# Kernel tuning notes

Hardware: AMD Instinct MI355X
Metric: run time of the kernel (lower is better)

The kernel has to match this reference:

```python
import jax, jax.numpy as jnp
import numpy as np

B, S, F = 4, 2048, 512
H, DH, OUT = 8, 64, 512  # attention_dim=512 -> head_dim=64
NEG_SLOPE = 0.01


def setup_inputs() -> dict:
    key = jax.random.key(0)
    ks = jax.random.split(key, 9)
    sc_in = 1.0 / np.sqrt(F)
    sc_hd = 1.0 / np.sqrt(H * DH)
    return {
        "x": jax.random.normal(ks[0], (B, S, F), dtype=jnp.float32),
        "Wq": jax.random.normal(ks[1], (F, H, DH), dtype=jnp.float32) * sc_in,
        "bq": jnp.zeros((H, DH), dtype=jnp.float32),
        "Wk": jax.random.normal(ks[2], (F, H, DH), dtype=jnp.float32) * sc_in,
        "bk": jnp.zeros((H, DH), dtype=jnp.float32),
        "Wv": jax.random.normal(ks[3], (F, H, DH), dtype=jnp.float32) * sc_in,
        "bv": jnp.zeros((H, DH), dtype=jnp.float32),
        "Wo": jax.random.normal(ks[4], (H, DH, OUT), dtype=jnp.float32) * sc_hd,
        "bo": jnp.zeros((OUT,), dtype=jnp.float32),
    }


def reference(x, Wq, bq, Wk, bk, Wv, bv, Wo, bo):
    # QKV projections: DenseGeneral(axis=-1, features=(H, DH)) -> [B, S, H, DH]
    q = jnp.einsum('bsf,fhd->bshd', x, Wq) + bq
    k = jnp.einsum('bsf,fhd->bshd', x, Wk) + bk
    v = jnp.einsum('bsf,fhd->bshd', x, Wv) + bv

    # Pairwise squared L2: l2[b,h,i,j] = ||q[b,i,h]-k[b,j,h]||^2
    q2 = jnp.sum(q * q, axis=-1)              # [B, S, H]
    k2 = jnp.sum(k * k, axis=-1)              # [B, S, H]
    qk = jnp.einsum('bihd,bjhd->bhij', q, k)  # [B, H, S, S]
    l2 = (q2.transpose(0, 2, 1)[:, :, :, None]
          + k2.transpose(0, 2, 1)[:, :, None, :]
          - 2.0 * qk)

    # softmax over key axis j, then weights.T @ value (note the transpose:
    # output token index is j, summed over query index i, as in the original)
    w = jax.nn.softmax(-l2, axis=-1)                  # [B, H, Si, Sj]
    attn = jnp.einsum('bhij,bihd->bjhd', w, v)        # [B, S, H, DH]

    # out DenseGeneral contracting (H, DH)
    out = jnp.einsum('bshd,hdo->bso', attn, Wo) + bo
    return jnp.where(out >= 0, out, NEG_SLOPE * out)
```

## Files before the change

### kernel.cpp

```cpp
#include <hip/hip_runtime.h>


typedef __attribute__((ext_vector_type(8))) short bf16x8;
typedef __attribute__((ext_vector_type(4))) float f32x4;
typedef __attribute__((ext_vector_type(4))) unsigned short u16x4;

#define MFMA16 __builtin_amdgcn_mfma_f32_16x16x32_bf16
#define LOG2E 1.4426950408889634f
#define TWO_LOG2E 2.8853900817779268f

__device__ inline unsigned short f2bf(float f) {
  unsigned int u = __float_as_uint(f);
  unsigned int r = 0x7fffu + ((u >> 16) & 1u);
  return (unsigned short)((u + r) >> 16);
}
__device__ inline float bf2f(unsigned short h) {
  return __uint_as_float(((unsigned int)h) << 16);
}
__device__ inline float fexp2(float x) { return __builtin_amdgcn_exp2f(x); }

__device__ inline void gl_lds16(const unsigned short* g, unsigned short* lds) {
  __builtin_amdgcn_global_load_lds(
      (const __attribute__((address_space(1))) unsigned int*)g,
      (__attribute__((address_space(3))) unsigned int*)lds, 16, 0, 0);
}

#define NXB4 (8192*512/4)
#define NWQ (1536*512)
#define NWO (512*512)

__global__ __launch_bounds__(256) void prep(
    const float* __restrict__ x, const float* __restrict__ Wq,
    const float* __restrict__ Wk, const float* __restrict__ Wv,
    const float* __restrict__ Wo, const float* __restrict__ bq,
    const float* __restrict__ bk, const float* __restrict__ bv,
    unsigned short* __restrict__ xb, unsigned short* __restrict__ wqkvT,
    unsigned short* __restrict__ woT, float* __restrict__ biasp) {
  int i = blockIdx.x * blockDim.x + threadIdx.x;
  if (i < NXB4) {
    f32x4 v = ((const f32x4*)x)[i];
    u16x4 o;
    o.x = f2bf(v.x); o.y = f2bf(v.y); o.z = f2bf(v.z); o.w = f2bf(v.w);
    ((u16x4*)xb)[i] = o;
    return;
  }
  i -= NXB4;
  if (i < NWQ) {
    int n = i >> 9, f = i & 511;
    const float* W = (n < 512) ? Wq : (n < 1024) ? Wk : Wv;
    wqkvT[i] = f2bf(W[f * 512 + (n & 511)]);
    return;
  }
  i -= NWQ;
  if (i < NWO) {
    int o = i >> 9, hd = i & 511;
    woT[i] = f2bf(Wo[hd * 512 + o]);
    return;
  }
  i -= NWO;
  if (i < 1536) {
    biasp[i] = (i < 512) ? bq[i] : (i < 1024) ? bk[i - 512] : bv[i - 1024];
  }
}

template<int MODE>
__global__ __launch_bounds__(256) void gemm_bt(
    const unsigned short* __restrict__ A, const unsigned short* __restrict__ Bt,
    const float* __restrict__ bias,
    unsigned short* __restrict__ o_q, unsigned short* __restrict__ o_k,
    unsigned short* __restrict__ o_v, float* __restrict__ o_f, int K) {
  const int m0 = blockIdx.y * 128;
  const int n0 = blockIdx.x * 128;
  const int tid = threadIdx.x;
  const int w = tid >> 6, l = tid & 63, lg = l >> 4, ll = l & 15;
  const int wr = w >> 1, wc = w & 1;
  __shared__ unsigned short a_lds[128 * 32];
  __shared__ unsigned short b_lds[128 * 32];
  f32x4 acc[4][4] = {};
  const int nkt = K >> 5;
  for (int kt = 0; kt < nkt; ++kt) {
#pragma unroll
    for (int c = 0; c < 2; ++c) {
      const int cc_base = c * 256 + w * 64;
      const int cc = cc_base + l;
      const int row = cc >> 2, cl = cc & 3;
      gl_lds16(A + (size_t)(m0 + row) * K + kt * 32 + cl * 8, a_lds + cc_base * 8);
      gl_lds16(Bt + (size_t)(n0 + row) * K + kt * 32 + cl * 8, b_lds + cc_base * 8);
    }
    __syncthreads();
    bf16x8 af[4], bfr[4];
#pragma unroll
    for (int mi = 0; mi < 4; ++mi)
      af[mi] = *(const bf16x8*)(a_lds + (wr * 64 + mi * 16 + ll) * 32 + lg * 8);
#pragma unroll
    for (int ni = 0; ni < 4; ++ni)
      bfr[ni] = *(const bf16x8*)(b_lds + (wc * 64 + ni * 16 + ll) * 32 + lg * 8);
#pragma unroll
    for (int mi = 0; mi < 4; ++mi)
#pragma unroll
      for (int ni = 0; ni < 4; ++ni)
        acc[mi][ni] = MFMA16(af[mi], bfr[ni], acc[mi][ni], 0, 0, 0);
    __syncthreads();
  }
#pragma unroll
  for (int mi = 0; mi < 4; ++mi)
#pragma unroll
    for (int ni = 0; ni < 4; ++ni) {
      const int col = n0 + wc * 64 + ni * 16 + ll;
      const float bb = bias[col];
#pragma unroll
      for (int r = 0; r < 4; ++r) {
        const int row = m0 + wr * 64 + mi * 16 + lg * 4 + r;
        float v = acc[mi][ni][r] + bb;
        if (MODE == 0) {
          const int which = col >> 9, h = (col >> 6) & 7, d = col & 63;
          const int b = row >> 11, s = row & 2047;
          if (which == 0) v *= TWO_LOG2E;
          const size_t idx = ((size_t)((b * 8 + h) * 2048 + s)) * 64 + d;
          (which == 0 ? o_q : which == 1 ? o_k : o_v)[idx] = f2bf(v);
        } else {
          v = v >= 0.f ? v : 0.01f * v;
          o_f[(size_t)row * 512 + col] = v;
        }
      }
    }
}

__global__ __launch_bounds__(256) void k2_kernel(const unsigned short* __restrict__ k_g,
                                                 float* __restrict__ k2l_g) {
  const int lane = threadIdx.x & 63;
  const int wid = (blockIdx.x * blockDim.x + threadIdx.x) >> 6;
  const int nw = (gridDim.x * blockDim.x) >> 6;
  for (int row = wid; row < 32 * 2048; row += nw) {
    float v = bf2f(k_g[(size_t)row * 64 + lane]);
    v *= v;
#pragma unroll
    for (int m = 1; m < 64; m <<= 1) v += __shfl_xor(v, m);
    if (lane == 0) k2l_g[row] = LOG2E * v;
  }
}

__global__ __launch_bounds__(256) void transpose_v(const unsigned short* __restrict__ v_g,
                                                   const float* __restrict__ invl_g,
                                                   unsigned short* __restrict__ vt_g) {
  const int bh = blockIdx.x >> 5, st = blockIdx.x & 31;
  const int s0 = st * 64;
  __shared__ unsigned short tile[64][72];
  const int t = threadIdx.x;
  {
    const int sl = t >> 2, cg = t & 3;
    const float sc = invl_g[bh * 2048 + s0 + sl];
    const unsigned short* src = v_g + ((size_t)(bh * 2048 + s0 + sl)) * 64 + cg * 16;
    bf16x8 v0 = *(const bf16x8*)(src);
    bf16x8 v1 = *(const bf16x8*)(src + 8);
#pragma unroll
    for (int e = 0; e < 8; ++e) tile[sl][cg * 16 + e] = f2bf(sc * bf2f((unsigned short)v0[e]));
#pragma unroll
    for (int e = 0; e < 8; ++e) tile[sl][cg * 16 + 8 + e] = f2bf(sc * bf2f((unsigned short)v1[e]));
  }
  __syncthreads();
  {
    const int dl = t >> 2, sg = t & 3;
    bf16x8 o0, o1;
#pragma unroll
    for (int e = 0; e < 8; ++e) o0[e] = (short)tile[sg * 16 + e][dl];
#pragma unroll
    for (int e = 0; e < 8; ++e) o1[e] = (short)tile[sg * 16 + 8 + e][dl];
    unsigned short* dst = vt_g + ((size_t)(bh * 64 + dl)) * 2048 + s0 + sg * 16;
    *(bf16x8*)dst = o0;
    *(bf16x8*)(dst + 8) = o1;
  }
}

__global__ __launch_bounds__(256) void pass1(const unsigned short* __restrict__ q_g,
                                             const unsigned short* __restrict__ k_g,
                                             const float* __restrict__ k2l_g,
                                             float* __restrict__ invl_g) {
  const int bh = blockIdx.x >> 5, ib = blockIdx.x & 31;
  const int i0 = ib * 64;
  const int tid = threadIdx.x, w = tid >> 6, l = tid & 63, lg = l >> 4, ll = l & 15;
  __shared__ unsigned short k_lds[64 * 64];
  __shared__ float k2_lds[64];
  const unsigned short* qrow = q_g + ((size_t)(bh * 2048 + i0 + w * 16 + ll)) * 64;
  const bf16x8 qa0 = *(const bf16x8*)(qrow + lg * 8);
  const bf16x8 qa1 = *(const bf16x8*)(qrow + 32 + lg * 8);
  float lrun[4] = {0.f, 0.f, 0.f, 0.f};
  for (int jt = 0; jt < 32; ++jt) {
    const int j0 = jt * 64;
#pragma unroll
    for (int c = 0; c < 2; ++c) {
      const int cc_base = c * 256 + w * 64;
      const int cc = cc_base + l;
      const int row = cc >> 3, cl = cc & 7;
      gl_lds16(k_g + ((size_t)(bh * 2048 + j0 + row)) * 64 + ((cl ^ (row & 7)) * 8),
               k_lds + cc_base * 8);
    }
    if (tid < 64) k2_lds[tid] = k2l_g[bh * 2048 + j0 + tid];
    __syncthreads();
#pragma unroll
    for (int nf = 0; nf < 4; ++nf) {
      const int jr = nf * 16 + ll;
      const unsigned short* kb = k_lds + jr * 64;
      const int sw = jr & 7;
      bf16x8 b0 = *(const bf16x8*)(kb + ((lg ^ sw) * 8));
      bf16x8 b1 = *(const bf16x8*)(kb + (((4 + lg) ^ sw) * 8));
      f32x4 sa = {};
      sa = MFMA16(qa0, b0, sa, 0, 0, 0);
      sa = MFMA16(qa1, b1, sa, 0, 0, 0);
      const float k2v = k2_lds[jr];
      lrun[0] += fexp2(sa[0] - k2v);
      lrun[1] += fexp2(sa[1] - k2v);
      lrun[2] += fexp2(sa[2] - k2v);
      lrun[3] += fexp2(sa[3] - k2v);
    }
    __syncthreads();
  }
#pragma unroll
  for (int r = 0; r < 4; ++r) {
    float t = lrun[r];
#pragma unroll
    for (int m = 1; m < 16; m <<= 1) t += __shfl_xor(t, m);
    if (ll == 0) invl_g[bh * 2048 + i0 + w * 16 + lg * 4 + r] = 1.f / t;
  }
}

__global__ __launch_bounds__(256) void pass2(const unsigned short* __restrict__ q_g,
                                             const unsigned short* __restrict__ k_g,
                                             const unsigned short* __restrict__ vt_g,
                                             const float* __restrict__ k2l_g,
                                             unsigned short* __restrict__ attnb) {
  const int bh = blockIdx.x >> 4, jb = blockIdx.x & 15;
  const int j0 = jb * 128;
  const int tid = threadIdx.x, w = tid >> 6, l = tid & 63, lg = l >> 4, ll = l & 15;
  __shared__ unsigned short q_lds[2][64 * 64];
  __shared__ unsigned short vt_lds[2][64 * 64];
  __shared__ unsigned short p_lds[128 * 64];
  const unsigned short* q_base = q_g + (size_t)bh * 2048 * 64;
  const unsigned short* vt_base = vt_g + (size_t)bh * 64 * 2048;
  const unsigned short* krow = k_g + ((size_t)(bh * 2048 + j0 + w * 32 + ll)) * 64;
  const bf16x8 ka00 = *(const bf16x8*)(krow + lg * 8);
  const bf16x8 ka01 = *(const bf16x8*)(krow + 32 + lg * 8);
  const bf16x8 ka10 = *(const bf16x8*)(krow + 1024 + lg * 8);
  const bf16x8 ka11 = *(const bf16x8*)(krow + 1024 + 32 + lg * 8);
  float k2v0[4], k2v1[4];
#pragma unroll
  for (int r = 0; r < 4; ++r) {
    k2v0[r] = k2l_g[bh * 2048 + j0 + w * 32 + lg * 4 + r];
    k2v1[r] = k2l_g[bh * 2048 + j0 + w * 32 + 16 + lg * 4 + r];
  }
  f32x4 oacc0[4] = {};
  f32x4 oacc1[4] = {};
#pragma unroll
  for (int c = 0; c < 2; ++c) {
    const int cc_base = c * 256 + w * 64;
    const int cc = cc_base + l;
    const int row = cc >> 3, cl = cc & 7;
    const int csw = (cl ^ (row & 7)) * 8;
    gl_lds16(q_base + (size_t)row * 64 + csw, &q_lds[0][cc_base * 8]);
    gl_lds16(vt_base + (size_t)row * 2048 + csw, &vt_lds[0][cc_base * 8]);
  }
  __syncthreads();
  for (int it = 0; it < 32; ++it) {
    const int slot = it & 1;
    if (it + 1 < 32) {
      const int i1 = (it + 1) * 64;
#pragma unroll
      for (int c = 0; c < 2; ++c) {
        const int cc_base = c * 256 + w * 64;
        const int cc = cc_base + l;
        const int row = cc >> 3, cl = cc & 7;
        const int csw = (cl ^ (row & 7)) * 8;
        gl_lds16(q_base + (size_t)(i1 + row) * 64 + csw, &q_lds[slot ^ 1][cc_base * 8]);
        gl_lds16(vt_base + (size_t)row * 2048 + i1 + csw, &vt_lds[slot ^ 1][cc_base * 8]);
      }
    }
#pragma unroll
    for (int nf = 0; nf < 4; ++nf) {
      const int ir = nf * 16 + ll;
      const unsigned short* qb = &q_lds[slot][ir * 64];
      const int sw = ir & 7;
      bf16x8 b0 = *(const bf16x8*)(qb + ((lg ^ sw) * 8));
      bf16x8 b1 = *(const bf16x8*)(qb + (((4 + lg) ^ sw) * 8));
      f32x4 sa0 = {};
      sa0 = MFMA16(ka00, b0, sa0, 0, 0, 0);
      sa0 = MFMA16(ka01, b1, sa0, 0, 0, 0);
      f32x4 sa1 = {};
      sa1 = MFMA16(ka10, b0, sa1, 0, 0, 0);
      sa1 = MFMA16(ka11, b1, sa1, 0, 0, 0);
#pragma unroll
      for (int r = 0; r < 4; ++r) {
        const float p0 = fexp2(sa0[r] - k2v0[r]);
        const float p1 = fexp2(sa1[r] - k2v1[r]);
        const int ja = w * 32 + lg * 4 + r;
        const int jb2 = ja + 16;
        p_lds[ja * 64 + (ir ^ ((ja & 7) << 3))] =
            (unsigned short)(__float_as_uint(p0) >> 16);
        p_lds[jb2 * 64 + (ir ^ ((jb2 & 7) << 3))] =
            (unsigned short)(__float_as_uint(p1) >> 16);
      }
    }
    {
      const int jr0 = w * 32 + ll;
      const int jr1 = jr0 + 16;
      const int swp = ll & 7;
      const unsigned short* pb0 = p_lds + jr0 * 64;
      const unsigned short* pb1 = p_lds + jr1 * 64;
      bf16x8 pa00 = *(const bf16x8*)(pb0 + ((lg ^ swp) * 8));
      bf16x8 pa01 = *(const bf16x8*)(pb0 + (((4 + lg) ^ swp) * 8));
      bf16x8 pa10 = *(const bf16x8*)(pb1 + ((lg ^ swp) * 8));
      bf16x8 pa11 = *(const bf16x8*)(pb1 + (((4 + lg) ^ swp) * 8));
#pragma unroll
      for (int nf = 0; nf < 4; ++nf) {
        const int dr = nf * 16 + ll;
        const unsigned short* vb = &vt_lds[slot][dr * 64];
        const int sw = dr & 7;
        bf16x8 v0 = *(const bf16x8*)(vb + ((lg ^ sw) * 8));
        bf16x8 v1 = *(const bf16x8*)(vb + (((4 + lg) ^ sw) * 8));
        oacc0[nf] = MFMA16(pa00, v0, oacc0[nf], 0, 0, 0);
        oacc0[nf] = MFMA16(pa01, v1, oacc0[nf], 0, 0, 0);
        oacc1[nf] = MFMA16(pa10, v0, oacc1[nf], 0, 0, 0);
        oacc1[nf] = MFMA16(pa11, v1, oacc1[nf], 0, 0, 0);
      }
    }
    __syncthreads();
  }
  const int b = bh >> 3, h2 = bh & 7;
#pragma unroll
  for (int nf = 0; nf < 4; ++nf) {
    const int d = nf * 16 + ll;
#pragma unroll
    for (int r = 0; r < 4; ++r) {
      const int j = j0 + w * 32 + lg * 4 + r;
      attnb[((size_t)(b * 2048 + j)) * 512 + h2 * 64 + d] = f2bf(oacc0[nf][r]);
      attnb[((size_t)(b * 2048 + j + 16)) * 512 + h2 * 64 + d] = f2bf(oacc1[nf][r]);
    }
  }
}

extern "C" void kernel_launch(void* const* d_in, const int* in_sizes, int n_in,
                              void* d_out, int out_size, void* d_ws, size_t ws_size,
                              hipStream_t stream) {
  const float* x  = (const float*)d_in[0];
  const float* Wq = (const float*)d_in[1];
  const float* bq = (const float*)d_in[2];
  const float* Wk = (const float*)d_in[3];
  const float* bk = (const float*)d_in[4];
  const float* Wv = (const float*)d_in[5];
  const float* bv = (const float*)d_in[6];
  const float* Wo = (const float*)d_in[7];
  const float* bo = (const float*)d_in[8];
  float* out = (float*)d_out;
  char* ws = (char*)d_ws;

  unsigned short* xb    = (unsigned short*)(ws);
  unsigned short* wqkvT = (unsigned short*)(ws + 8388608);
  unsigned short* woT   = (unsigned short*)(ws + 9961472);
  float*          biasp = (float*)         (ws + 10485760);
  unsigned short* q_g   = (unsigned short*)(ws + 10493952);
  unsigned short* k_g   = (unsigned short*)(ws + 18882560);
  unsigned short* v_g   = (unsigned short*)(ws + 27271168);
  unsigned short* vt_g  = (unsigned short*)(ws + 35659776);
  float*          k2_g  = (float*)         (ws + 44048384);
  float*          invl_g= (float*)         (ws + 44310528);
  unsigned short* attnb = (unsigned short*)(ws + 44572672);
  if (ws_size < (size_t)52961280) return;

  prep<<<8199, 256, 0, stream>>>(x, Wq, Wk, Wv, Wo, bq, bk, bv, xb, wqkvT, woT, biasp);
  gemm_bt<0><<<dim3(12, 64), 256, 0, stream>>>(xb, wqkvT, biasp, q_g, k_g, v_g, nullptr, 512);
  k2_kernel<<<1024, 256, 0, stream>>>(k_g, k2_g);
  pass1<<<1024, 256, 0, stream>>>(q_g, k_g, k2_g, invl_g);
  transpose_v<<<1024, 256, 0, stream>>>(v_g, invl_g, vt_g);
  pass2<<<512, 256, 0, stream>>>(q_g, k_g, vt_g, k2_g, attnb);
  gemm_bt<1><<<dim3(4, 64), 256, 0, stream>>>(attnb, woT, bo, nullptr, nullptr, nullptr, out, 512);
}
```

Measured before the change: 165.0 us.

## Split pass2 over the query axis into two partials and double pass1 rows per block

pass2 now launches a second grid dimension that splits the 32 query tiles into two halves. Each half writes a bf16 partial, into attnb or into the reused xb buffer, and a new combine kernel adds the two. This doubles the number of pass2 blocks from 512 to 1024 to improve CU occupancy on the longest stage. pass1 is changed so each wave handles 32 query rows, sharing each K tile load across two MFMA row groups and halving its block count. The cost is an extra kernel launch and extra bf16 traffic for the partials, plus a second bf16 rounding on the attention output.

```diff
diff --git a/kernel.cpp b/kernel.cpp
--- a/kernel.cpp
+++ b/kernel.cpp
@@ -176,15 +176,18 @@
                                              const unsigned short* __restrict__ k_g,
                                              const float* __restrict__ k2l_g,
                                              float* __restrict__ invl_g) {
-  const int bh = blockIdx.x >> 5, ib = blockIdx.x & 31;
-  const int i0 = ib * 64;
+  const int bh = blockIdx.x >> 4, ib = blockIdx.x & 15;
+  const int i0 = ib * 128;
   const int tid = threadIdx.x, w = tid >> 6, l = tid & 63, lg = l >> 4, ll = l & 15;
   __shared__ unsigned short k_lds[64 * 64];
   __shared__ float k2_lds[64];
-  const unsigned short* qrow = q_g + ((size_t)(bh * 2048 + i0 + w * 16 + ll)) * 64;
-  const bf16x8 qa0 = *(const bf16x8*)(qrow + lg * 8);
-  const bf16x8 qa1 = *(const bf16x8*)(qrow + 32 + lg * 8);
-  float lrun[4] = {0.f, 0.f, 0.f, 0.f};
+  const unsigned short* qrow = q_g + ((size_t)(bh * 2048 + i0 + w * 32 + ll)) * 64;
+  const bf16x8 qa00 = *(const bf16x8*)(qrow + lg * 8);
+  const bf16x8 qa01 = *(const bf16x8*)(qrow + 32 + lg * 8);
+  const bf16x8 qa10 = *(const bf16x8*)(qrow + 1024 + lg * 8);
+  const bf16x8 qa11 = *(const bf16x8*)(qrow + 1024 + 32 + lg * 8);
+  float lrun0[4] = {0.f, 0.f, 0.f, 0.f};
+  float lrun1[4] = {0.f, 0.f, 0.f, 0.f};
   for (int jt = 0; jt < 32; ++jt) {
     const int j0 = jt * 64;
 #pragma unroll
@@ -204,23 +207,33 @@
       const int sw = jr & 7;
       bf16x8 b0 = *(const bf16x8*)(kb + ((lg ^ sw) * 8));
       bf16x8 b1 = *(const bf16x8*)(kb + (((4 + lg) ^ sw) * 8));
-      f32x4 sa = {};
-      sa = MFMA16(qa0, b0, sa, 0, 0, 0);
-      sa = MFMA16(qa1, b1, sa, 0, 0, 0);
+      f32x4 sa0 = {};
+      sa0 = MFMA16(qa00, b0, sa0, 0, 0, 0);
+      sa0 = MFMA16(qa01, b1, sa0, 0, 0, 0);
+      f32x4 sa1 = {};
+      sa1 = MFMA16(qa10, b0, sa1, 0, 0, 0);
+      sa1 = MFMA16(qa11, b1, sa1, 0, 0, 0);
       const float k2v = k2_lds[jr];
-      lrun[0] += fexp2(sa[0] - k2v);
-      lrun[1] += fexp2(sa[1] - k2v);
-      lrun[2] += fexp2(sa[2] - k2v);
-      lrun[3] += fexp2(sa[3] - k2v);
+      lrun0[0] += fexp2(sa0[0] - k2v);
+      lrun0[1] += fexp2(sa0[1] - k2v);
+      lrun0[2] += fexp2(sa0[2] - k2v);
+      lrun0[3] += fexp2(sa0[3] - k2v);
+      lrun1[0] += fexp2(sa1[0] - k2v);
+      lrun1[1] += fexp2(sa1[1] - k2v);
+      lrun1[2] += fexp2(sa1[2] - k2v);
+      lrun1[3] += fexp2(sa1[3] - k2v);
     }
     __syncthreads();
   }
 #pragma unroll
   for (int r = 0; r < 4; ++r) {
-    float t = lrun[r];
-#pragma unroll
-    for (int m = 1; m < 16; m <<= 1) t += __shfl_xor(t, m);
-    if (ll == 0) invl_g[bh * 2048 + i0 + w * 16 + lg * 4 + r] = 1.f / t;
+    float t0 = lrun0[r], t1 = lrun1[r];
+#pragma unroll
+    for (int m = 1; m < 16; m <<= 1) { t0 += __shfl_xor(t0, m); t1 += __shfl_xor(t1, m); }
+    if (ll == 0) {
+      invl_g[bh * 2048 + i0 + w * 32 + lg * 4 + r] = 1.f / t0;
+      invl_g[bh * 2048 + i0 + w * 32 + 16 + lg * 4 + r] = 1.f / t1;
+    }
   }
 }
 
@@ -228,9 +241,12 @@
                                              const unsigned short* __restrict__ k_g,
                                              const unsigned short* __restrict__ vt_g,
                                              const float* __restrict__ k2l_g,
-                                             unsigned short* __restrict__ attnb) {
+                                             unsigned short* __restrict__ part0,
+                                             unsigned short* __restrict__ part1) {
   const int bh = blockIdx.x >> 4, jb = blockIdx.x & 15;
+  const int by = blockIdx.y;
   const int j0 = jb * 128;
+  const int it0 = by << 4, it_end = it0 + 16;
   const int tid = threadIdx.x, w = tid >> 6, l = tid & 63, lg = l >> 4, ll = l & 15;
   __shared__ unsigned short q_lds[2][64 * 64];
   __shared__ unsigned short vt_lds[2][64 * 64];
@@ -256,13 +272,13 @@
     const int cc = cc_base + l;
     const int row = cc >> 3, cl = cc & 7;
     const int csw = (cl ^ (row & 7)) * 8;
-    gl_lds16(q_base + (size_t)row * 64 + csw, &q_lds[0][cc_base * 8]);
-    gl_lds16(vt_base + (size_t)row * 2048 + csw, &vt_lds[0][cc_base * 8]);
+    gl_lds16(q_base + (size_t)(it0 * 64 + row) * 64 + csw, &q_lds[0][cc_base * 8]);
+    gl_lds16(vt_base + (size_t)row * 2048 + it0 * 64 + csw, &vt_lds[0][cc_base * 8]);
   }
   __syncthreads();
-  for (int it = 0; it < 32; ++it) {
+  for (int it = it0; it < it_end; ++it) {
     const int slot = it & 1;
-    if (it + 1 < 32) {
+    if (it + 1 < it_end) {
       const int i1 = (it + 1) * 64;
 #pragma unroll
       for (int c = 0; c < 2; ++c) {
@@ -324,6 +340,7 @@
     }
     __syncthreads();
   }
+  unsigned short* po = by ? part1 : part0;
   const int b = bh >> 3, h2 = bh & 7;
 #pragma unroll
   for (int nf = 0; nf < 4; ++nf) {
@@ -331,10 +348,22 @@
 #pragma unroll
     for (int r = 0; r < 4; ++r) {
       const int j = j0 + w * 32 + lg * 4 + r;
-      attnb[((size_t)(b * 2048 + j)) * 512 + h2 * 64 + d] = f2bf(oacc0[nf][r]);
-      attnb[((size_t)(b * 2048 + j + 16)) * 512 + h2 * 64 + d] = f2bf(oacc1[nf][r]);
-    }
-  }
+      po[((size_t)(b * 2048 + j)) * 512 + h2 * 64 + d] = f2bf(oacc0[nf][r]);
+      po[((size_t)(b * 2048 + j + 16)) * 512 + h2 * 64 + d] = f2bf(oacc1[nf][r]);
+    }
+  }
+}
+
+__global__ __launch_bounds__(256) void combine(unsigned short* __restrict__ p0,
+                                               const unsigned short* __restrict__ p1) {
+  const int i = blockIdx.x * blockDim.x + threadIdx.x;
+  bf16x8 a = ((const bf16x8*)p0)[i];
+  bf16x8 b = ((const bf16x8*)p1)[i];
+  bf16x8 o;
+#pragma unroll
+  for (int e = 0; e < 8; ++e)
+    o[e] = (short)f2bf(bf2f((unsigned short)a[e]) + bf2f((unsigned short)b[e]));
+  ((bf16x8*)p0)[i] = o;
 }
 
 extern "C" void kernel_launch(void* const* d_in, const int* in_sizes, int n_in,
@@ -368,8 +397,9 @@
   prep<<<8199, 256, 0, stream>>>(x, Wq, Wk, Wv, Wo, bq, bk, bv, xb, wqkvT, woT, biasp);
   gemm_bt<0><<<dim3(12, 64), 256, 0, stream>>>(xb, wqkvT, biasp, q_g, k_g, v_g, nullptr, 512);
   k2_kernel<<<1024, 256, 0, stream>>>(k_g, k2_g);
-  pass1<<<1024, 256, 0, stream>>>(q_g, k_g, k2_g, invl_g);
+  pass1<<<512, 256, 0, stream>>>(q_g, k_g, k2_g, invl_g);
   transpose_v<<<1024, 256, 0, stream>>>(v_g, invl_g, vt_g);
-  pass2<<<512, 256, 0, stream>>>(q_g, k_g, vt_g, k2_g, attnb);
+  pass2<<<dim3(512, 2), 256, 0, stream>>>(q_g, k_g, vt_g, k2_g, attnb, xb);
+  combine<<<2048, 256, 0, stream>>>(attnb, xb);
   gemm_bt<1><<<dim3(4, 64), 256, 0, stream>>>(attnb, woT, bo, nullptr, nullptr, nullptr, out, 512);
 }
```

Result: no change. 161.9 us (-1.9%).
